# Performance work log

Measured on AMD Instinct MI355X. Metric: run time of the kernel, lower is better.

Reference implementation:

```python
import jax, jax.numpy as jnp
import numpy as np

TEMPERATURE = 0.07
EPS = 1e-8  # torch F.cosine_similarity eps


def setup_inputs() -> dict:
    key = jax.random.key(0)
    k1, k2 = jax.random.split(key)
    N, D = 4096, 256
    z1 = jax.random.normal(k1, (N, D), dtype=jnp.float32)
    z2 = jax.random.normal(k2, (N, D), dtype=jnp.float32)
    return {"z1": z1, "z2": z2}


def reference(z1, z2):
    N = z1.shape[0]
    z = jnp.concatenate([z1, z2], axis=0)  # (2N, D)
    # cosine similarity = normalize(z) @ normalize(z).T (with eps clamp on norms)
    norms = jnp.maximum(jnp.linalg.norm(z, axis=-1, keepdims=True), EPS)
    zn = z / norms
    sim = (zn @ zn.T) / TEMPERATURE  # (2N, 2N)
    twoN = 2 * N
    eye = jnp.eye(twoN, dtype=bool)
    sim = jnp.where(eye, -1e9, sim)
    pos = jnp.concatenate([jnp.arange(N, twoN), jnp.arange(0, N)])
    # cross entropy with integer targets, mean reduction
    logZ = jax.nn.logsumexp(sim, axis=-1)  # (2N,)
    pos_logit = jnp.take_along_axis(sim, pos[:, None], axis=1)[:, 0]
    loss = jnp.mean(logZ - pos_logit)
    return loss
```

## Files before the change

kernel.cpp:

```cpp
#include <hip/hip_runtime.h>

#define N2   8192
#define NTRI 2080

static constexpr float INV_T = 1.0f / 0.07f;

using f32x4 = __attribute__((ext_vector_type(4))) float;
using i32x4 = __attribute__((ext_vector_type(4))) int;
using i32x8 = __attribute__((ext_vector_type(8))) int;
typedef unsigned int u32;

#define GL2LDS(gp, lp) __builtin_amdgcn_global_load_lds( \
    (const __attribute__((address_space(1))) void*)(gp), \
    (__attribute__((address_space(3))) void*)(lp), 16, 0, 0)

#define SCALE1 0x7F7F7F7F

__global__ void ntx_norm(const float* __restrict__ z1, const float* __restrict__ z2,
                         unsigned char* __restrict__ zn)
{
    const int w    = threadIdx.x >> 6;
    const int lane = threadIdx.x & 63;
    const int row  = blockIdx.x * 4 + w;

    const float* src = (row < 4096) ? (z1 + (size_t)row * 256)
                                    : (z2 + (size_t)(row - 4096) * 256);
    float4 v = *(const float4*)(src + lane * 4);
    float ss = v.x * v.x + v.y * v.y + v.z * v.z + v.w * v.w;
    #pragma unroll
    for (int m = 1; m < 64; m <<= 1) ss += __shfl_xor(ss, m, 64);

    float inv = 1.0f / fmaxf(sqrtf(ss), 1e-8f);

    u32 p = __builtin_amdgcn_cvt_pk_fp8_f32(v.x * inv, v.y * inv, 0u, false);
    p     = __builtin_amdgcn_cvt_pk_fp8_f32(v.z * inv, v.w * inv, p, true);
    ((u32*)zn)[(size_t)row * 64 + lane] = p;
}

__global__ __launch_bounds__(256, 3)
void ntx_gemm(const unsigned char* __restrict__ zn, float* __restrict__ partials,
              float* __restrict__ pos)
{
    __shared__ __align__(16) unsigned char lsA[16384];
    __shared__ __align__(16) unsigned char lsB[16384];

    const int tid  = threadIdx.x;
    const int lane = tid & 63;
    const int w    = tid >> 6;
    const int wr   = w >> 1;
    const int wc   = w & 1;

    const int t = (int)blockIdx.x;
    int br = (int)((129.0f - sqrtf(16641.0f - 8.0f * (float)t)) * 0.5f);
    while ((br + 1) * (129 - (br + 1)) / 2 <= t) ++br;
    while (br * (129 - br) / 2 > t) --br;
    const int bc = br + (t - br * (129 - br) / 2);

    const int fr  = lane & 15;
    const int kl  = lane >> 4;
    const int swz = (fr & 7) << 4;

    const int srow = w * 8 + (lane >> 3);
    const int scsw = ((lane & 7) * 16) ^ ((lane >> 3) << 4);

    auto stage = [&](int kt) {
        const char* gA = (const char*)zn + (size_t)(br * 128 + srow) * 256 + kt * 128 + scsw;
        const char* gB = (const char*)zn + (size_t)(bc * 128 + srow) * 256 + kt * 128 + scsw;
        #pragma unroll
        for (int i = 0; i < 4; ++i) {
            GL2LDS(gA + (size_t)i * 8192, lsA + i * 4096 + w * 1024);
            GL2LDS(gB + (size_t)i * 8192, lsB + i * 4096 + w * 1024);
        }
    };

    f32x4 acc[4][4] = {};

    auto compute = [&]() {
        const int kb = kl * 32;
        i32x8 af[4], bv[4];
        #pragma unroll
        for (int mf = 0; mf < 4; ++mf) {
            const int r = wr * 64 + mf * 16 + fr;
            const char* base = (const char*)lsA + r * 128;
            i32x4 lo = *(const i32x4*)(base + ((kb)      ^ swz));
            i32x4 hi = *(const i32x4*)(base + ((kb + 16) ^ swz));
            af[mf] = (i32x8){lo[0], lo[1], lo[2], lo[3], hi[0], hi[1], hi[2], hi[3]};
        }
        #pragma unroll
        for (int nf = 0; nf < 4; ++nf) {
            const int c = wc * 64 + nf * 16 + fr;
            const char* base = (const char*)lsB + c * 128;
            i32x4 lo = *(const i32x4*)(base + ((kb)      ^ swz));
            i32x4 hi = *(const i32x4*)(base + ((kb + 16) ^ swz));
            bv[nf] = (i32x8){lo[0], lo[1], lo[2], lo[3], hi[0], hi[1], hi[2], hi[3]};
        }
        __builtin_amdgcn_s_setprio(1);
        #pragma unroll
        for (int mf = 0; mf < 4; ++mf)
            #pragma unroll
            for (int nf = 0; nf < 4; ++nf)
                acc[mf][nf] = __builtin_amdgcn_mfma_scale_f32_16x16x128_f8f6f4(
                    af[mf], bv[nf], acc[mf][nf], 0, 0, 0, SCALE1, 0, SCALE1);
        __builtin_amdgcn_s_setprio(0);
    };

    stage(0);
    __syncthreads();
    compute();
    __syncthreads();
    stage(1);
    __syncthreads();
    compute();

    const bool offdiag = (br != bc);
    const bool posblk  = (bc == br + 32);
    float colsum[4] = {0.f, 0.f, 0.f, 0.f};

    #pragma unroll
    for (int mf = 0; mf < 4; ++mf) {
        float rs[4] = {0.f, 0.f, 0.f, 0.f};
        const int rowq = br * 128 + wr * 64 + mf * 16 + kl * 4;
        #pragma unroll
        for (int nf = 0; nf < 4; ++nf) {
            const int col = bc * 128 + wc * 64 + nf * 16 + fr;
            f32x4 a = acc[mf][nf];
            #pragma unroll
            for (int j = 0; j < 4; ++j) {
                float e = (rowq + j == col) ? 0.f : __expf((a[j] - 1.0f) * INV_T);
                rs[j]      += e;
                colsum[nf] += e;
                if (posblk && (rowq + j + 4096 == col)) {
                    pos[rowq + j] = a[j];
                    pos[col]      = a[j];
                }
            }
        }
        #pragma unroll
        for (int m = 1; m < 16; m <<= 1) {
            #pragma unroll
            for (int j = 0; j < 4; ++j) rs[j] += __shfl_xor(rs[j], m, 64);
        }
        if (fr == 0) {
            float* p = partials + (size_t)rowq * 128 + bc * 2 + wc;
            p[0]   = rs[0];
            p[128] = rs[1];
            p[256] = rs[2];
            p[384] = rs[3];
        }
    }

    if (offdiag) {
        #pragma unroll
        for (int m = 16; m < 64; m <<= 1) {
            #pragma unroll
            for (int nf = 0; nf < 4; ++nf) colsum[nf] += __shfl_xor(colsum[nf], m, 64);
        }
        if (kl == 0) {
            #pragma unroll
            for (int nf = 0; nf < 4; ++nf) {
                const int col = bc * 128 + wc * 64 + nf * 16 + fr;
                partials[(size_t)col * 128 + br * 2 + wr] = colsum[nf];
            }
        }
    }
}

__global__ void ntx_loss(const float* __restrict__ partials, const float* __restrict__ pos,
                         float* __restrict__ bsums, u32* __restrict__ counter,
                         float* __restrict__ out)
{
    __shared__ float sm[16];
    __shared__ u32 flag;
    const int tid  = threadIdx.x;
    const int lane = tid & 63;
    const int w    = tid >> 6;

    float a = 0.f;
    #pragma unroll
    for (int i = 0; i < 8; ++i) {
        const int row = blockIdx.x * 128 + w * 8 + i;
        float S = partials[(size_t)row * 128 + lane] + partials[(size_t)row * 128 + 64 + lane];
        #pragma unroll
        for (int m = 1; m < 64; m <<= 1) S += __shfl_xor(S, m, 64);
        if (lane == 0) a += __logf(S) + INV_T - pos[row] * INV_T;
    }
    if (lane == 0) sm[w] = a;
    __syncthreads();

    if (tid == 0) {
        float b = 0.f;
        #pragma unroll
        for (int i = 0; i < 16; ++i) b += sm[i];
        bsums[blockIdx.x] = b;
        __threadfence();
        u32 old = atomicAdd(counter, 1u);
        flag = (old == 63u) ? 1u : 0u;
    }
    __syncthreads();

    if (flag && w == 0) {
        __threadfence();
        float v = bsums[lane];
        #pragma unroll
        for (int m = 1; m < 64; m <<= 1) v += __shfl_xor(v, m, 64);
        if (lane == 0) out[0] = v * (1.0f / (float)N2);
    }
}

extern "C" void kernel_launch(void* const* d_in, const int* in_sizes, int n_in,
                              void* d_out, int out_size, void* d_ws, size_t ws_size,
                              hipStream_t stream)
{
    const float* z1 = (const float*)d_in[0];
    const float* z2 = (const float*)d_in[1];
    float* out = (float*)d_out;

    unsigned char* zn       = (unsigned char*)d_ws;
    float*         partials = (float*)((char*)d_ws + (2u << 20));
    float*         pos      = (float*)((char*)d_ws + (6u << 20));
    float*         bsums    = pos + N2;
    u32*           counter  = (u32*)(bsums + 64);

    hipMemsetAsync(counter, 0, 4, stream);
    ntx_norm<<<N2 / 4, 256, 0, stream>>>(z1, z2, zn);
    ntx_gemm<<<NTRI, 256, 0, stream>>>(zn, partials, pos);
    ntx_loss<<<64, 1024, 0, stream>>>(partials, pos, bsums, counter, out);
}
```

Measured before the change: 48.14 us.

## Load GEMM fragments directly from global memory and fold counter reset into norm kernel

The GEMM kernel stops staging A and B tiles through LDS with global_load_lds and barriers. Each wave now reads its MFMA fragments straight from global memory, relying on L1/L2 to absorb the duplicated reads across waves, and the launch-bounds occupancy hint is relaxed. Separately, the hipMemsetAsync that reset the atomic counter is removed and the reset moves into the norm kernel, saving one launch. This trades LDS sharing and synchronisation for redundant global loads that may be less coalesced.

```diff
diff --git a/kernel.cpp b/kernel.cpp
--- a/kernel.cpp
+++ b/kernel.cpp
@@ -10,15 +10,13 @@
 using i32x8 = __attribute__((ext_vector_type(8))) int;
 typedef unsigned int u32;
 
-#define GL2LDS(gp, lp) __builtin_amdgcn_global_load_lds( \
-    (const __attribute__((address_space(1))) void*)(gp), \
-    (__attribute__((address_space(3))) void*)(lp), 16, 0, 0)
-
 #define SCALE1 0x7F7F7F7F
 
 __global__ void ntx_norm(const float* __restrict__ z1, const float* __restrict__ z2,
-                         unsigned char* __restrict__ zn)
-{
+                         unsigned char* __restrict__ zn, u32* __restrict__ counter)
+{
+    if (blockIdx.x == 0 && threadIdx.x == 0) *counter = 0;
+
     const int w    = threadIdx.x >> 6;
     const int lane = threadIdx.x & 63;
     const int row  = blockIdx.x * 4 + w;
@@ -37,13 +35,10 @@
     ((u32*)zn)[(size_t)row * 64 + lane] = p;
 }
 
-__global__ __launch_bounds__(256, 3)
+__global__ __launch_bounds__(256)
 void ntx_gemm(const unsigned char* __restrict__ zn, float* __restrict__ partials,
               float* __restrict__ pos)
 {
-    __shared__ __align__(16) unsigned char lsA[16384];
-    __shared__ __align__(16) unsigned char lsB[16384];
-
     const int tid  = threadIdx.x;
     const int lane = tid & 63;
     const int w    = tid >> 6;
@@ -56,42 +51,29 @@
     while (br * (129 - br) / 2 > t) --br;
     const int bc = br + (t - br * (129 - br) / 2);
 
-    const int fr  = lane & 15;
-    const int kl  = lane >> 4;
-    const int swz = (fr & 7) << 4;
-
-    const int srow = w * 8 + (lane >> 3);
-    const int scsw = ((lane & 7) * 16) ^ ((lane >> 3) << 4);
-
-    auto stage = [&](int kt) {
-        const char* gA = (const char*)zn + (size_t)(br * 128 + srow) * 256 + kt * 128 + scsw;
-        const char* gB = (const char*)zn + (size_t)(bc * 128 + srow) * 256 + kt * 128 + scsw;
-        #pragma unroll
-        for (int i = 0; i < 4; ++i) {
-            GL2LDS(gA + (size_t)i * 8192, lsA + i * 4096 + w * 1024);
-            GL2LDS(gB + (size_t)i * 8192, lsB + i * 4096 + w * 1024);
-        }
-    };
+    const int fr = lane & 15;
+    const int kl = lane >> 4;
+
+    const char* baseA = (const char*)zn + (size_t)(br * 128 + wr * 64 + fr) * 256 + kl * 32;
+    const char* baseB = (const char*)zn + (size_t)(bc * 128 + wc * 64 + fr) * 256 + kl * 32;
 
     f32x4 acc[4][4] = {};
 
-    auto compute = [&]() {
-        const int kb = kl * 32;
+    #pragma unroll
+    for (int kt = 0; kt < 2; ++kt) {
         i32x8 af[4], bv[4];
         #pragma unroll
         for (int mf = 0; mf < 4; ++mf) {
-            const int r = wr * 64 + mf * 16 + fr;
-            const char* base = (const char*)lsA + r * 128;
-            i32x4 lo = *(const i32x4*)(base + ((kb)      ^ swz));
-            i32x4 hi = *(const i32x4*)(base + ((kb + 16) ^ swz));
+            const char* p = baseA + mf * 4096 + kt * 128;
+            i32x4 lo = *(const i32x4*)(p);
+            i32x4 hi = *(const i32x4*)(p + 16);
             af[mf] = (i32x8){lo[0], lo[1], lo[2], lo[3], hi[0], hi[1], hi[2], hi[3]};
         }
         #pragma unroll
         for (int nf = 0; nf < 4; ++nf) {
-            const int c = wc * 64 + nf * 16 + fr;
-            const char* base = (const char*)lsB + c * 128;
-            i32x4 lo = *(const i32x4*)(base + ((kb)      ^ swz));
-            i32x4 hi = *(const i32x4*)(base + ((kb + 16) ^ swz));
+            const char* p = baseB + nf * 4096 + kt * 128;
+            i32x4 lo = *(const i32x4*)(p);
+            i32x4 hi = *(const i32x4*)(p + 16);
             bv[nf] = (i32x8){lo[0], lo[1], lo[2], lo[3], hi[0], hi[1], hi[2], hi[3]};
         }
         __builtin_amdgcn_s_setprio(1);
@@ -102,15 +84,7 @@
                 acc[mf][nf] = __builtin_amdgcn_mfma_scale_f32_16x16x128_f8f6f4(
                     af[mf], bv[nf], acc[mf][nf], 0, 0, 0, SCALE1, 0, SCALE1);
         __builtin_amdgcn_s_setprio(0);
-    };
-
-    stage(0);
-    __syncthreads();
-    compute();
-    __syncthreads();
-    stage(1);
-    __syncthreads();
-    compute();
+    }
 
     const bool offdiag = (br != bc);
     const bool posblk  = (bc == br + 32);
@@ -221,8 +195,7 @@
     float*         bsums    = pos + N2;
     u32*           counter  = (u32*)(bsums + 64);
 
-    hipMemsetAsync(counter, 0, 4, stream);
-    ntx_norm<<<N2 / 4, 256, 0, stream>>>(z1, z2, zn);
+    ntx_norm<<<N2 / 4, 256, 0, stream>>>(z1, z2, zn, counter);
     ntx_gemm<<<NTRI, 256, 0, stream>>>(zn, partials, pos);
     ntx_loss<<<64, 1024, 0, stream>>>(partials, pos, bsums, counter, out);
 }
```

Result: slower. 61.27 us (+27.3%).
